# Performance work log

Measured on AMD Instinct MI355X. Metric: run time of the kernel, lower is better.

## Reference

```python
import jax, jax.numpy as jnp
import numpy as np

N, D, B, E, K, H, C = 100000, 256, 20000, 16, 3, 256, 40  # m = K = 3


def setup_inputs() -> dict:
    key = jax.random.key(0)
    ks = jax.random.split(key, 11)
    return {
        "nodes": jax.random.randint(ks[0], (B,), 0, N, dtype=jnp.int32),
        "structure": jax.random.randint(ks[1], (B, E, K), 0, N, dtype=jnp.int32),
        "X": jax.random.normal(ks[2], (N, D), dtype=jnp.float32),
        "beta": jax.random.uniform(ks[3], (1,), dtype=jnp.float32),
        "w_att_w": jax.random.normal(ks[4], (1,), dtype=jnp.float32),
        "w_att_b": jax.random.normal(ks[5], (1,), dtype=jnp.float32),
        "lin_W": jax.random.normal(ks[6], (H, D), dtype=jnp.float32) * 0.05,
        "lin_b": jax.random.normal(ks[7], (H,), dtype=jnp.float32) * 0.05,
        "skip_W": jax.random.normal(ks[8], (H, D), dtype=jnp.float32) * 0.05,
        "cls_W": jax.random.normal(ks[9], (C, H), dtype=jnp.float32) * 0.05,
        "cls_b": jax.random.normal(ks[10], (C,), dtype=jnp.float32) * 0.05,
    }


def reference(nodes, structure, X, beta, w_att_w, w_att_b, lin_W, lin_b, skip_W, cls_W, cls_b):
    # --- TMessagePassing (batched over nodes and hyperedges) ---
    feats = X[structure]                                  # [B, E, K, D] gather
    # variance over nodes in the hyperedge (unbiased=False), mean over feature dim
    edge_var = jnp.var(feats, axis=2).mean(axis=-1)       # [B, E]
    att = jax.nn.sigmoid(w_att_w[0] * edge_var + w_att_b[0])  # [B, E]
    # len(edge) == m (K == m=3): msg = prod(feats[:-1], dim=0)
    msg = jnp.prod(feats[:, :, : K - 1, :], axis=2)       # [B, E, D]
    neigh = jnp.einsum("be,bed->bd", att, msg)            # sum of att * msg over edges
    # --- Encoder (combine == 'sum') ---
    self_feat = X[nodes]                                  # [B, D]
    h = self_feat + neigh
    enc = jax.nn.relu(h @ lin_W.T + lin_b)                # [B, H]
    enc = (1.0 - beta[0]) * enc + beta[0] * (self_feat @ skip_W.T)
    # --- classifier + log_softmax ---
    logits = enc @ cls_W.T + cls_b                        # [B, C]
    return jax.nn.log_softmax(logits, axis=1)
```

## Files before the change

### kernel.cpp

```cpp
#include <hip/hip_runtime.h>
#include <hip/hip_bf16.h>
#include <math.h>

#define Dn 256
#define En 16
#define Kn 3
#define Hn 256
#define Cn 40
#define CnP 48

typedef __attribute__((ext_vector_type(8)))  short bf16x8;
typedef __attribute__((ext_vector_type(4)))  float f32x4;

static __device__ __forceinline__ float bf2f(unsigned short u) {
    return __uint_as_float(((unsigned)u) << 16);
}
static __device__ __forceinline__ unsigned short f2bfbits(float v) {
    __hip_bfloat16 hb = __float2bfloat16(v);
    return *reinterpret_cast<unsigned short*>(&hb);
}
static __device__ __forceinline__ unsigned pack2bf(float a, float b) {
    return (unsigned)f2bfbits(a) | ((unsigned)f2bfbits(b) << 16);
}
static __device__ __forceinline__ unsigned swz4(unsigned boff) {
    return boff ^ (((boff >> 9) & 15u) << 4);
}

__global__ __launch_bounds__(256) void conv_all(
    const float* __restrict__ X, const float* __restrict__ linW,
    const float* __restrict__ skipW, const float* __restrict__ clsW,
    uint4* __restrict__ Xb, uint4* __restrict__ linWb,
    uint4* __restrict__ skipWb, uint4* __restrict__ clsWb,
    int x8, int w8)
{
    int t = blockIdx.x * 256 + threadIdx.x;
    const int c8 = (CnP * Hn) / 8;
    if (t < x8) {
        const float4* iv = reinterpret_cast<const float4*>(X);
        const float4 a = iv[(size_t)t * 2 + 0];
        const float4 b = iv[(size_t)t * 2 + 1];
        Xb[t] = (uint4){pack2bf(a.x, a.y), pack2bf(a.z, a.w),
                        pack2bf(b.x, b.y), pack2bf(b.z, b.w)};
        return;
    }
    t -= x8;
    if (t < w8) {
        const float4* iv = reinterpret_cast<const float4*>(linW);
        const float4 a = iv[(size_t)t * 2 + 0];
        const float4 b = iv[(size_t)t * 2 + 1];
        linWb[t] = (uint4){pack2bf(a.x, a.y), pack2bf(a.z, a.w),
                           pack2bf(b.x, b.y), pack2bf(b.z, b.w)};
        return;
    }
    t -= w8;
    if (t < w8) {
        const float4* iv = reinterpret_cast<const float4*>(skipW);
        const float4 a = iv[(size_t)t * 2 + 0];
        const float4 b = iv[(size_t)t * 2 + 1];
        skipWb[t] = (uint4){pack2bf(a.x, a.y), pack2bf(a.z, a.w),
                            pack2bf(b.x, b.y), pack2bf(b.z, b.w)};
        return;
    }
    t -= w8;
    if (t < c8) {
        const int row = t >> 5;
        if (row < Cn) {
            const float4* iv = reinterpret_cast<const float4*>(clsW);
            const float4 a = iv[(size_t)t * 2 + 0];
            const float4 b = iv[(size_t)t * 2 + 1];
            clsWb[t] = (uint4){pack2bf(a.x, a.y), pack2bf(a.z, a.w),
                               pack2bf(b.x, b.y), pack2bf(b.z, b.w)};
        } else {
            clsWb[t] = (uint4){0u, 0u, 0u, 0u};
        }
    }
}

__global__ __launch_bounds__(256) void mp_kernel_bf(
    const int* __restrict__ nodes, const int* __restrict__ structure,
    const uint2* __restrict__ Xb,
    const float* __restrict__ waw_p, const float* __restrict__ wab_p,
    uint2* __restrict__ h_out, uint2* __restrict__ self_out, int B)
{
    const int wave = threadIdx.x >> 6;
    const int lane = threadIdx.x & 63;
    const int b = blockIdx.x * 4 + wave;
    if (b >= B) return;
    const int ub = __builtin_amdgcn_readfirstlane(b);

    const float waw = waw_p[0];
    const float wab = wab_p[0];

    float4 neigh = make_float4(0.f, 0.f, 0.f, 0.f);
    const int* st = structure + (size_t)ub * (En * Kn);

    #pragma unroll 1
    for (int g = 0; g < En / 4; ++g) {
        int idx[12];
        #pragma unroll
        for (int u = 0; u < 12; ++u) idx[u] = st[g * 12 + u];

        uint2 r0[4], r1[4], r2[4];
        #pragma unroll
        for (int u = 0; u < 4; ++u) {
            r0[u] = Xb[(size_t)idx[u * 3 + 0] * (Dn / 4) + lane];
            r1[u] = Xb[(size_t)idx[u * 3 + 1] * (Dn / 4) + lane];
            r2[u] = Xb[(size_t)idx[u * 3 + 2] * (Dn / 4) + lane];
        }

        float pv[4];
        float4 msg[4];
        #pragma unroll
        for (int u = 0; u < 4; ++u) {
            float4 f0, f1, f2;
            f0.x = bf2f((unsigned short)(r0[u].x & 0xffff));
            f0.y = bf2f((unsigned short)(r0[u].x >> 16));
            f0.z = bf2f((unsigned short)(r0[u].y & 0xffff));
            f0.w = bf2f((unsigned short)(r0[u].y >> 16));
            f1.x = bf2f((unsigned short)(r1[u].x & 0xffff));
            f1.y = bf2f((unsigned short)(r1[u].x >> 16));
            f1.z = bf2f((unsigned short)(r1[u].y & 0xffff));
            f1.w = bf2f((unsigned short)(r1[u].y >> 16));
            f2.x = bf2f((unsigned short)(r2[u].x & 0xffff));
            f2.y = bf2f((unsigned short)(r2[u].x >> 16));
            f2.z = bf2f((unsigned short)(r2[u].y & 0xffff));
            f2.w = bf2f((unsigned short)(r2[u].y >> 16));

            float s2 = 0.f, cr = 0.f, tt;
            s2 = fmaf(f0.x, f0.x, s2); s2 = fmaf(f1.x, f1.x, s2); s2 = fmaf(f2.x, f2.x, s2);
            tt = f1.x + f2.x; cr = fmaf(f0.x, tt, cr); cr = fmaf(f1.x, f2.x, cr);
            s2 = fmaf(f0.y, f0.y, s2); s2 = fmaf(f1.y, f1.y, s2); s2 = fmaf(f2.y, f2.y, s2);
            tt = f1.y + f2.y; cr = fmaf(f0.y, tt, cr); cr = fmaf(f1.y, f2.y, cr);
            s2 = fmaf(f0.z, f0.z, s2); s2 = fmaf(f1.z, f1.z, s2); s2 = fmaf(f2.z, f2.z, s2);
            tt = f1.z + f2.z; cr = fmaf(f0.z, tt, cr); cr = fmaf(f1.z, f2.z, cr);
            s2 = fmaf(f0.w, f0.w, s2); s2 = fmaf(f1.w, f1.w, s2); s2 = fmaf(f2.w, f2.w, s2);
            tt = f1.w + f2.w; cr = fmaf(f0.w, tt, cr); cr = fmaf(f1.w, f2.w, cr);

            pv[u] = s2 - cr;
            msg[u].x = f0.x * f1.x;
            msg[u].y = f0.y * f1.y;
            msg[u].z = f0.z * f1.z;
            msg[u].w = f0.w * f1.w;
        }

        #pragma unroll
        for (int off = 32; off; off >>= 1) {
            #pragma unroll
            for (int u = 0; u < 4; ++u) pv[u] += __shfl_xor(pv[u], off);
        }

        #pragma unroll
        for (int u = 0; u < 4; ++u) {
            const float var_mean = pv[u] * (2.f / (9.f * (float)Dn));
            const float att = 1.f / (1.f + expf(-(waw * var_mean + wab)));
            neigh.x += att * msg[u].x;
            neigh.y += att * msg[u].y;
            neigh.z += att * msg[u].z;
            neigh.w += att * msg[u].w;
        }
    }

    const uint2 sv = Xb[(size_t)nodes[ub] * (Dn / 4) + lane];
    self_out[(size_t)b * (Dn / 4) + lane] = sv;
    const float sx = bf2f((unsigned short)(sv.x & 0xffff));
    const float sy = bf2f((unsigned short)(sv.x >> 16));
    const float sz = bf2f((unsigned short)(sv.y & 0xffff));
    const float sw = bf2f((unsigned short)(sv.y >> 16));
    uint2 o;
    o.x = pack2bf(sx + neigh.x, sy + neigh.y);
    o.y = pack2bf(sz + neigh.z, sw + neigh.w);
    h_out[(size_t)b * (Dn / 4) + lane] = o;
}

__global__ __launch_bounds__(256, 4) void enc_cls16(
    const unsigned short* __restrict__ hB,
    const unsigned short* __restrict__ selfB,
    const unsigned short* __restrict__ linWb, const float* __restrict__ linb,
    const unsigned short* __restrict__ skipWb, const float* __restrict__ beta_p,
    const unsigned short* __restrict__ clsWb,
    const float* __restrict__ clsb,
    float* __restrict__ out, int M)
{
    __shared__ unsigned short elds[16 * 256];

    const int w    = threadIdx.x >> 6;
    const int l    = threadIdx.x & 63;
    const int lr16 = l & 15;
    const int kg   = l >> 4;
    const int row0 = blockIdx.x * 16;

    const int arow = row0 + lr16;
    const int arc  = arow < M ? arow : (M - 1);

    f32x4 acc1[4], acc2[4];
    #pragma unroll
    for (int n = 0; n < 4; ++n) {
        acc1[n] = (f32x4){0.f, 0.f, 0.f, 0.f};
        acc2[n] = (f32x4){0.f, 0.f, 0.f, 0.f};
    }

    #pragma unroll 2
    for (int k0 = 0; k0 < Dn; k0 += 32) {
        const int ko = k0 + kg * 8;
        const bf16x8 a1 = *reinterpret_cast<const bf16x8*>(hB    + (size_t)arc * Dn + ko);
        const bf16x8 a2 = *reinterpret_cast<const bf16x8*>(selfB + (size_t)arc * Dn + ko);
        #pragma unroll
        for (int n = 0; n < 4; ++n) {
            const int col = w * 64 + n * 16 + lr16;
            const bf16x8 b1 = *reinterpret_cast<const bf16x8*>(linWb  + (size_t)col * Dn + ko);
            const bf16x8 b2 = *reinterpret_cast<const bf16x8*>(skipWb + (size_t)col * Dn + ko);
            acc1[n] = __builtin_amdgcn_mfma_f32_16x16x32_bf16(a1, b1, acc1[n], 0, 0, 0);
            acc2[n] = __builtin_amdgcn_mfma_f32_16x16x32_bf16(a2, b2, acc2[n], 0, 0, 0);
        }
    }

    const float beta = beta_p[0];
    const float omb = 1.f - beta;
    #pragma unroll
    for (int n = 0; n < 4; ++n) {
        const int col = w * 64 + n * 16 + lr16;
        const float bias = linb[col];
        #pragma unroll
        for (int r = 0; r < 4; ++r) {
            const int rowl = kg * 4 + r;
            const float c1 = fmaxf(acc1[n][r] + bias, 0.f);
            const unsigned short v = f2bfbits(omb * c1 + beta * acc2[n][r]);
            const unsigned boff = swz4((unsigned)(rowl * 512 + col * 2));
            *reinterpret_cast<unsigned short*>(
                reinterpret_cast<char*>(elds) + boff) = v;
        }
    }
    __syncthreads();

    if (w == 0) {
        f32x4 cacc[3];
        cacc[0] = (f32x4){0.f,0.f,0.f,0.f};
        cacc[1] = (f32x4){0.f,0.f,0.f,0.f};
        cacc[2] = (f32x4){0.f,0.f,0.f,0.f};

        #pragma unroll
        for (int k0 = 0; k0 < Hn; k0 += 32) {
            const int ko = k0 + kg * 8;
            const unsigned boff = swz4((unsigned)(lr16 * 512 + ko * 2));
            const bf16x8 a = *reinterpret_cast<const bf16x8*>(
                reinterpret_cast<const char*>(elds) + boff);
            #pragma unroll
            for (int t = 0; t < 3; ++t) {
                const bf16x8 bb = *reinterpret_cast<const bf16x8*>(
                    clsWb + (size_t)(t * 16 + lr16) * Hn + ko);
                cacc[t] = __builtin_amdgcn_mfma_f32_16x16x32_bf16(a, bb, cacc[t], 0, 0, 0);
            }
        }

        float bias3[3];
        #pragma unroll
        for (int t = 0; t < 3; ++t) {
            const int cb = t * 16 + lr16;
            bias3[t] = (cb < Cn) ? clsb[cb] : -INFINITY;
        }

        #pragma unroll
        for (int r = 0; r < 4; ++r) {
            float lg0 = cacc[0][r] + bias3[0];
            float lg1 = cacc[1][r] + bias3[1];
            float lg2 = cacc[2][r] + bias3[2];
            float mx = fmaxf(fmaxf(lg0, lg1), lg2);
            #pragma unroll
            for (int off = 8; off; off >>= 1) mx = fmaxf(mx, __shfl_xor(mx, off));
            float se = expf(lg0 - mx) + expf(lg1 - mx) + expf(lg2 - mx);
            #pragma unroll
            for (int off = 8; off; off >>= 1) se += __shfl_xor(se, off);
            const float lse = logf(se);

            const int row = row0 + kg * 4 + r;
            if (row < M) {
                if (lr16 < 8) out[(size_t)row * Cn + 32 + lr16] = lg2 - mx - lse;
                out[(size_t)row * Cn + lr16]      = lg0 - mx - lse;
                out[(size_t)row * Cn + 16 + lr16] = lg1 - mx - lse;
            }
        }
    }
}

__global__ __launch_bounds__(256) void mp_kernel_f32(
    const int* __restrict__ nodes, const int* __restrict__ structure,
    const float* __restrict__ X, const float* __restrict__ waw_p,
    const float* __restrict__ wab_p, float* __restrict__ h_out, int B)
{
    const int wave = threadIdx.x >> 6;
    const int lane = threadIdx.x & 63;
    const int b = blockIdx.x * 4 + wave;
    if (b >= B) return;
    const int ub = __builtin_amdgcn_readfirstlane(b);

    const float waw = waw_p[0];
    const float wab = wab_p[0];
    const float4* __restrict__ Xv = reinterpret_cast<const float4*>(X);

    float4 neigh = make_float4(0.f, 0.f, 0.f, 0.f);
    const int* st = structure + (size_t)ub * (En * Kn);

    #pragma unroll 1
    for (int e = 0; e < En; ++e) {
        const int i0 = st[e * 3 + 0];
        const int i1 = st[e * 3 + 1];
        const int i2 = st[e * 3 + 2];
        const float4 f0 = Xv[(size_t)i0 * (Dn / 4) + lane];
        const float4 f1 = Xv[(size_t)i1 * (Dn / 4) + lane];
        const float4 f2 = Xv[(size_t)i2 * (Dn / 4) + lane];
        float pv = 0.f;
        {
            float a, bb, c, m;
            a = f0.x; bb = f1.x; c = f2.x;
            m = (a + bb + c) * (1.f / 3.f);
            pv += (a * a + bb * bb + c * c) * (1.f / 3.f) - m * m;
            a = f0.y; bb = f1.y; c = f2.y;
            m = (a + bb + c) * (1.f / 3.f);
            pv += (a * a + bb * bb + c * c) * (1.f / 3.f) - m * m;
            a = f0.z; bb = f1.z; c = f2.z;
            m = (a + bb + c) * (1.f / 3.f);
            pv += (a * a + bb * bb + c * c) * (1.f / 3.f) - m * m;
            a = f0.w; bb = f1.w; c = f2.w;
            m = (a + bb + c) * (1.f / 3.f);
            pv += (a * a + bb * bb + c * c) * (1.f / 3.f) - m * m;
        }
        #pragma unroll
        for (int off = 32; off; off >>= 1) pv += __shfl_xor(pv, off);
        const float var_mean = pv * (1.f / (float)Dn);
        const float att = 1.f / (1.f + expf(-(waw * var_mean + wab)));
        neigh.x += att * f0.x * f1.x;
        neigh.y += att * f0.y * f1.y;
        neigh.z += att * f0.z * f1.z;
        neigh.w += att * f0.w * f1.w;
    }

    const float4 s = Xv[(size_t)nodes[ub] * (Dn / 4) + lane];
    float4 h;
    h.x = s.x + neigh.x; h.y = s.y + neigh.y;
    h.z = s.z + neigh.z; h.w = s.w + neigh.w;
    reinterpret_cast<float4*>(h_out)[(size_t)b * (Dn / 4) + lane] = h;
}

#define BM 64
#define BN 64
#define BKs 16
#define LDT 68

__global__ __launch_bounds__(256) void enc_gemm_f32(
    const float* __restrict__ hA, const int* __restrict__ nodes,
    const float* __restrict__ X,
    const float* __restrict__ linW, const float* __restrict__ linb,
    const float* __restrict__ skipW, const float* __restrict__ beta_p,
    float* __restrict__ enc2, int M)
{
    __shared__ float Ats1[BKs][LDT];
    __shared__ float Ats2[BKs][LDT];
    __shared__ float Bts1[BKs][LDT];
    __shared__ float Bts2[BKs][LDT];

    const int tid = threadIdx.x;
    const int tx = tid & 15;
    const int ty = tid >> 4;
    const int row0 = blockIdx.x * BM;
    const int col0 = blockIdx.y * BN;

    const int lr = tid >> 2;
    const int lc = tid & 3;

    const int arow = row0 + lr;
    const bool arow_ok = arow < M;
    const int self_row = arow_ok ? nodes[arow] : 0;

    float acc1[4][4] = {{0.f}}, acc2[4][4] = {{0.f}};

    for (int k0 = 0; k0 < Dn; k0 += BKs) {
        float4 a1v = make_float4(0.f, 0.f, 0.f, 0.f);
        float4 a2v = make_float4(0.f, 0.f, 0.f, 0.f);
        if (arow_ok) {
            a1v = *reinterpret_cast<const float4*>(hA + (size_t)arow * Dn + k0 + lc * 4);
            a2v = *reinterpret_cast<const float4*>(X + (size_t)self_row * Dn + k0 + lc * 4);
        }
        const float4 b1v = *reinterpret_cast<const float4*>(linW + (size_t)(col0 + lr) * Dn + k0 + lc * 4);
        const float4 b2v = *reinterpret_cast<const float4*>(skipW + (size_t)(col0 + lr) * Dn + k0 + lc * 4);

        __syncthreads();
        Ats1[lc * 4 + 0][lr] = a1v.x; Ats1[lc * 4 + 1][lr] = a1v.y;
        Ats1[lc * 4 + 2][lr] = a1v.z; Ats1[lc * 4 + 3][lr] = a1v.w;
        Ats2[lc * 4 + 0][lr] = a2v.x; Ats2[lc * 4 + 1][lr] = a2v.y;
        Ats2[lc * 4 + 2][lr] = a2v.z; Ats2[lc * 4 + 3][lr] = a2v.w;
        Bts1[lc * 4 + 0][lr] = b1v.x; Bts1[lc * 4 + 1][lr] = b1v.y;
        Bts1[lc * 4 + 2][lr] = b1v.z; Bts1[lc * 4 + 3][lr] = b1v.w;
        Bts2[lc * 4 + 0][lr] = b2v.x; Bts2[lc * 4 + 1][lr] = b2v.y;
        Bts2[lc * 4 + 2][lr] = b2v.z; Bts2[lc * 4 + 3][lr] = b2v.w;
        __syncthreads();

        #pragma unroll
        for (int kk = 0; kk < BKs; ++kk) {
            const float4 a1 = *reinterpret_cast<const float4*>(&Ats1[kk][ty * 4]);
            const float4 a2 = *reinterpret_cast<const float4*>(&Ats2[kk][ty * 4]);
            const float4 b1 = *reinterpret_cast<const float4*>(&Bts1[kk][tx * 4]);
            const float4 b2 = *reinterpret_cast<const float4*>(&Bts2[kk][tx * 4]);
            const float a1a[4] = {a1.x, a1.y, a1.z, a1.w};
            const float a2a[4] = {a2.x, a2.y, a2.z, a2.w};
            const float b1a[4] = {b1.x, b1.y, b1.z, b1.w};
            const float b2a[4] = {b2.x, b2.y, b2.z, b2.w};
            #pragma unroll
            for (int i = 0; i < 4; ++i)
                #pragma unroll
                for (int j = 0; j < 4; ++j) {
                    acc1[i][j] = fmaf(a1a[i], b1a[j], acc1[i][j]);
                    acc2[i][j] = fmaf(a2a[i], b2a[j], acc2[i][j]);
                }
        }
    }

    const float beta = beta_p[0];
    const float omb = 1.f - beta;
    #pragma unroll
    for (int i = 0; i < 4; ++i) {
        const int r = row0 + ty * 4 + i;
        if (r >= M) continue;
        #pragma unroll
        for (int j = 0; j < 4; ++j) {
            const int c = col0 + tx * 4 + j;
            float c1 = acc1[i][j] + linb[c];
            c1 = fmaxf(c1, 0.f);
            enc2[(size_t)r * Hn + c] = omb * c1 + beta * acc2[i][j];
        }
    }
}

__global__ __launch_bounds__(256) void cls_kernel_f32(
    const float* __restrict__ enc2, const float* __restrict__ clsW,
    const float* __restrict__ clsb, float* __restrict__ out, int B)
{
    const int wave = threadIdx.x >> 6;
    const int lane = threadIdx.x & 63;
    const int b = blockIdx.x * 4 + wave;
    if (b >= B) return;

    const float4 e = reinterpret_cast<const float4*>(enc2 + (size_t)b * Hn)[lane];
    const float4* __restrict__ clsWv = reinterpret_cast<const float4*>(clsW);

    float mylogit = -INFINITY;
    #pragma unroll
    for (int c0 = 0; c0 < Cn; c0 += 8) {
        float p[8];
        #pragma unroll
        for (int u = 0; u < 8; ++u) {
            const float4 wv = clsWv[(size_t)(c0 + u) * (Hn / 4) + lane];
            p[u] = e.x * wv.x + e.y * wv.y + e.z * wv.z + e.w * wv.w;
        }
        #pragma unroll
        for (int off = 32; off; off >>= 1) {
            #pragma unroll
            for (int u = 0; u < 8; ++u) p[u] += __shfl_xor(p[u], off);
        }
        #pragma unroll
        for (int u = 0; u < 8; ++u)
            if (lane == c0 + u) mylogit = p[u];
    }
    if (lane < Cn) mylogit += clsb[lane];

    float mx = mylogit;
    #pragma unroll
    for (int off = 32; off; off >>= 1) mx = fmaxf(mx, __shfl_xor(mx, off));
    float ex = (lane < Cn) ? expf(mylogit - mx) : 0.f;
    float se = ex;
    #pragma unroll
    for (int off = 32; off; off >>= 1) se += __shfl_xor(se, off);
    const float lse = logf(se);

    if (lane < Cn) out[(size_t)b * Cn + lane] = mylogit - mx - lse;
}

extern "C" void kernel_launch(void* const* d_in, const int* in_sizes, int n_in,
                              void* d_out, int out_size, void* d_ws, size_t ws_size,
                              hipStream_t stream) {
    const int*   nodes     = (const int*)d_in[0];
    const int*   structure = (const int*)d_in[1];
    const float* X         = (const float*)d_in[2];
    const float* beta      = (const float*)d_in[3];
    const float* waw       = (const float*)d_in[4];
    const float* wab       = (const float*)d_in[5];
    const float* linW      = (const float*)d_in[6];
    const float* linb      = (const float*)d_in[7];
    const float* skipW     = (const float*)d_in[8];
    const float* clsW      = (const float*)d_in[9];
    const float* clsb      = (const float*)d_in[10];
    float* out = (float*)d_out;

    const int B = in_sizes[0];
    const int Ntot = in_sizes[2];

    unsigned short* h_bf   = (unsigned short*)d_ws;
    unsigned short* selfb  = h_bf + (size_t)B * Dn;
    unsigned short* Xb     = selfb + (size_t)B * Dn;
    unsigned short* linWb  = Xb + (size_t)Ntot;
    unsigned short* skipWb = linWb + (size_t)Hn * Dn;
    unsigned short* clsWb  = skipWb + (size_t)Hn * Dn;

    const size_t need = ((size_t)B * Dn * 2 + (size_t)Ntot +
                         (size_t)Hn * Dn * 2 + (size_t)CnP * Hn) * 2;

    if (ws_size >= need) {
        const int x8 = Ntot / 8;
        const int w8 = (Hn * Dn) / 8;
        const int c8 = (CnP * Hn) / 8;
        const int G = x8 + 2 * w8 + c8;
        conv_all<<<(G + 255) / 256, 256, 0, stream>>>(
            X, linW, skipW, clsW,
            (uint4*)Xb, (uint4*)linWb, (uint4*)skipWb, (uint4*)clsWb, x8, w8);

        mp_kernel_bf<<<(B + 3) / 4, 256, 0, stream>>>(
            nodes, structure, (const uint2*)Xb, waw, wab,
            (uint2*)h_bf, (uint2*)selfb, B);

        enc_cls16<<<(B + 15) / 16, 256, 0, stream>>>(
            h_bf, selfb, linWb, linb, skipWb, beta, clsWb, clsb, out, B);
    } else {
        float* enc2 = (float*)d_ws;
        float* hf   = enc2 + (size_t)B * Hn;
        mp_kernel_f32<<<(B + 3) / 4, 256, 0, stream>>>(nodes, structure, X, waw, wab, hf, B);
        dim3 g2((B + BM - 1) / BM, Hn / BN);
        enc_gemm_f32<<<g2, 256, 0, stream>>>(hf, nodes, X, linW, linb, skipW, beta, enc2, B);
        cls_kernel_f32<<<(B + 3) / 4, 256, 0, stream>>>(enc2, clsW, clsb, out, B);
    }
}
```

Before: 148.5 us.

## Prepack weights into MFMA fragment order and stage activations in LDS

The weight conversion kernel now writes lin, skip and classifier weights in a packed per-fragment layout, so each wave's B-operand loads become contiguous 16-byte-per-lane reads instead of strided row accesses. The encoder kernel first copies the 16-row tiles of h and self features into swizzled LDS with coalesced loads, then reads the A fragments from LDS. This is meant to improve global load coalescing and avoid each of the four waves re-reading the same A rows from global memory. In exchange it adds 16 KB more LDS per block, which may lower occupancy, plus an extra barrier.

```diff
diff --git a/kernel.cpp b/kernel.cpp
--- a/kernel.cpp
+++ b/kernel.cpp
@@ -29,8 +29,8 @@
 __global__ __launch_bounds__(256) void conv_all(
     const float* __restrict__ X, const float* __restrict__ linW,
     const float* __restrict__ skipW, const float* __restrict__ clsW,
-    uint4* __restrict__ Xb, uint4* __restrict__ linWb,
-    uint4* __restrict__ skipWb, uint4* __restrict__ clsWb,
+    uint4* __restrict__ Xb, uint4* __restrict__ linWp,
+    uint4* __restrict__ skipWp, uint4* __restrict__ clsWp,
     int x8, int w8)
 {
     int t = blockIdx.x * 256 + threadIdx.x;
@@ -48,8 +48,11 @@
         const float4* iv = reinterpret_cast<const float4*>(linW);
         const float4 a = iv[(size_t)t * 2 + 0];
         const float4 b = iv[(size_t)t * 2 + 1];
-        linWb[t] = (uint4){pack2bf(a.x, a.y), pack2bf(a.z, a.w),
-                           pack2bf(b.x, b.y), pack2bf(b.z, b.w)};
+        const int lc = (t >> 5) & 15, ct = t >> 9;
+        const int kt = (t >> 2) & 7,  kg = t & 3;
+        linWp[(ct * 8 + kt) * 64 + kg * 16 + lc] =
+            (uint4){pack2bf(a.x, a.y), pack2bf(a.z, a.w),
+                    pack2bf(b.x, b.y), pack2bf(b.z, b.w)};
         return;
     }
     t -= w8;
@@ -57,21 +60,27 @@
         const float4* iv = reinterpret_cast<const float4*>(skipW);
         const float4 a = iv[(size_t)t * 2 + 0];
         const float4 b = iv[(size_t)t * 2 + 1];
-        skipWb[t] = (uint4){pack2bf(a.x, a.y), pack2bf(a.z, a.w),
-                            pack2bf(b.x, b.y), pack2bf(b.z, b.w)};
+        const int lc = (t >> 5) & 15, ct = t >> 9;
+        const int kt = (t >> 2) & 7,  kg = t & 3;
+        skipWp[(ct * 8 + kt) * 64 + kg * 16 + lc] =
+            (uint4){pack2bf(a.x, a.y), pack2bf(a.z, a.w),
+                    pack2bf(b.x, b.y), pack2bf(b.z, b.w)};
         return;
     }
     t -= w8;
     if (t < c8) {
-        const int row = t >> 5;
-        if (row < Cn) {
+        const int col = t >> 5;
+        const int lc = col & 15, ct = t >> 9;
+        const int kt = (t >> 2) & 7, kg = t & 3;
+        const int dst = (ct * 8 + kt) * 64 + kg * 16 + lc;
+        if (col < Cn) {
             const float4* iv = reinterpret_cast<const float4*>(clsW);
             const float4 a = iv[(size_t)t * 2 + 0];
             const float4 b = iv[(size_t)t * 2 + 1];
-            clsWb[t] = (uint4){pack2bf(a.x, a.y), pack2bf(a.z, a.w),
-                               pack2bf(b.x, b.y), pack2bf(b.z, b.w)};
+            clsWp[dst] = (uint4){pack2bf(a.x, a.y), pack2bf(a.z, a.w),
+                                 pack2bf(b.x, b.y), pack2bf(b.z, b.w)};
         } else {
-            clsWb[t] = (uint4){0u, 0u, 0u, 0u};
+            clsWp[dst] = (uint4){0u, 0u, 0u, 0u};
         }
     }
 }
@@ -175,12 +184,14 @@
 __global__ __launch_bounds__(256, 4) void enc_cls16(
     const unsigned short* __restrict__ hB,
     const unsigned short* __restrict__ selfB,
-    const unsigned short* __restrict__ linWb, const float* __restrict__ linb,
-    const unsigned short* __restrict__ skipWb, const float* __restrict__ beta_p,
-    const unsigned short* __restrict__ clsWb,
+    const uint4* __restrict__ linWp, const float* __restrict__ linb,
+    const uint4* __restrict__ skipWp, const float* __restrict__ beta_p,
+    const uint4* __restrict__ clsWp,
     const float* __restrict__ clsb,
     float* __restrict__ out, int M)
 {
+    __shared__ unsigned short hlds[16 * 256];
+    __shared__ unsigned short slds[16 * 256];
     __shared__ unsigned short elds[16 * 256];
 
     const int w    = threadIdx.x >> 6;
@@ -189,8 +200,20 @@
     const int kg   = l >> 4;
     const int row0 = blockIdx.x * 16;
 
-    const int arow = row0 + lr16;
-    const int arc  = arow < M ? arow : (M - 1);
+    #pragma unroll
+    for (int it = 0; it < 2; ++it) {
+        const int ch = it * 256 + threadIdx.x;
+        const int r  = ch >> 5;
+        const int c  = ch & 31;
+        int grow = row0 + r;
+        grow = grow < M ? grow : (M - 1);
+        const uint4 hv = *reinterpret_cast<const uint4*>(hB    + (size_t)grow * Dn + c * 8);
+        const uint4 sv = *reinterpret_cast<const uint4*>(selfB + (size_t)grow * Dn + c * 8);
+        const unsigned boff = swz4((unsigned)(r * 512 + c * 16));
+        *reinterpret_cast<uint4*>(reinterpret_cast<char*>(hlds) + boff) = hv;
+        *reinterpret_cast<uint4*>(reinterpret_cast<char*>(slds) + boff) = sv;
+    }
+    __syncthreads();
 
     f32x4 acc1[4], acc2[4];
     #pragma unroll
@@ -201,14 +224,17 @@
 
     #pragma unroll 2
     for (int k0 = 0; k0 < Dn; k0 += 32) {
-        const int ko = k0 + kg * 8;
-        const bf16x8 a1 = *reinterpret_cast<const bf16x8*>(hB    + (size_t)arc * Dn + ko);
-        const bf16x8 a2 = *reinterpret_cast<const bf16x8*>(selfB + (size_t)arc * Dn + ko);
+        const int kt = k0 >> 5;
+        const unsigned aoff = swz4((unsigned)(lr16 * 512 + k0 * 2 + kg * 16));
+        const bf16x8 a1 = *reinterpret_cast<const bf16x8*>(
+            reinterpret_cast<const char*>(hlds) + aoff);
+        const bf16x8 a2 = *reinterpret_cast<const bf16x8*>(
+            reinterpret_cast<const char*>(slds) + aoff);
         #pragma unroll
         for (int n = 0; n < 4; ++n) {
-            const int col = w * 64 + n * 16 + lr16;
-            const bf16x8 b1 = *reinterpret_cast<const bf16x8*>(linWb  + (size_t)col * Dn + ko);
-            const bf16x8 b2 = *reinterpret_cast<const bf16x8*>(skipWb + (size_t)col * Dn + ko);
+            const int fidx = ((w * 4 + n) * 8 + kt) * 64 + l;
+            const bf16x8 b1 = *reinterpret_cast<const bf16x8*>(linWp  + fidx);
+            const bf16x8 b2 = *reinterpret_cast<const bf16x8*>(skipWp + fidx);
             acc1[n] = __builtin_amdgcn_mfma_f32_16x16x32_bf16(a1, b1, acc1[n], 0, 0, 0);
             acc2[n] = __builtin_amdgcn_mfma_f32_16x16x32_bf16(a2, b2, acc2[n], 0, 0, 0);
         }
@@ -240,14 +266,14 @@
 
         #pragma unroll
         for (int k0 = 0; k0 < Hn; k0 += 32) {
-            const int ko = k0 + kg * 8;
-            const unsigned boff = swz4((unsigned)(lr16 * 512 + ko * 2));
+            const int kt = k0 >> 5;
+            const unsigned boff = swz4((unsigned)(lr16 * 512 + k0 * 2 + kg * 16));
             const bf16x8 a = *reinterpret_cast<const bf16x8*>(
                 reinterpret_cast<const char*>(elds) + boff);
             #pragma unroll
             for (int t = 0; t < 3; ++t) {
                 const bf16x8 bb = *reinterpret_cast<const bf16x8*>(
-                    clsWb + (size_t)(t * 16 + lr16) * Hn + ko);
+                    clsWp + ((t * 8 + kt) * 64 + l));
                 cacc[t] = __builtin_amdgcn_mfma_f32_16x16x32_bf16(a, bb, cacc[t], 0, 0, 0);
             }
         }
@@ -496,9 +522,9 @@
     unsigned short* h_bf   = (unsigned short*)d_ws;
     unsigned short* selfb  = h_bf + (size_t)B * Dn;
     unsigned short* Xb     = selfb + (size_t)B * Dn;
-    unsigned short* linWb  = Xb + (size_t)Ntot;
-    unsigned short* skipWb = linWb + (size_t)Hn * Dn;
-    unsigned short* clsWb  = skipWb + (size_t)Hn * Dn;
+    unsigned short* linWp  = Xb + (size_t)Ntot;
+    unsigned short* skipWp = linWp + (size_t)Hn * Dn;
+    unsigned short* clsWp  = skipWp + (size_t)Hn * Dn;
 
     const size_t need = ((size_t)B * Dn * 2 + (size_t)Ntot +
                          (size_t)Hn * Dn * 2 + (size_t)CnP * Hn) * 2;
@@ -510,14 +536,15 @@
         const int G = x8 + 2 * w8 + c8;
         conv_all<<<(G + 255) / 256, 256, 0, stream>>>(
             X, linW, skipW, clsW,
-            (uint4*)Xb, (uint4*)linWb, (uint4*)skipWb, (uint4*)clsWb, x8, w8);
+            (uint4*)Xb, (uint4*)linWp, (uint4*)skipWp, (uint4*)clsWp, x8, w8);
 
         mp_kernel_bf<<<(B + 3) / 4, 256, 0, stream>>>(
             nodes, structure, (const uint2*)Xb, waw, wab,
             (uint2*)h_bf, (uint2*)selfb, B);
 
         enc_cls16<<<(B + 15) / 16, 256, 0, stream>>>(
-            h_bf, selfb, linWb, linb, skipWb, beta, clsWb, clsb, out, B);
+            h_bf, selfb, (const uint4*)linWp, linb, (const uint4*)skipWp,
+            beta, (const uint4*)clsWp, clsb, out, B);
     } else {
         float* enc2 = (float*)d_ws;
         float* hf   = enc2 + (size_t)B * Hn;
```

Result: faster. 128.7 us (-13.3%).
